# Optimization experiments

Measured on AMD Instinct MI355X. Metric: run time of the kernel, lower is better.

## Reference

```python
import jax, jax.numpy as jnp
import numpy as np


def conv1x1(x, w, b):
    # 1x1 Conv2d: x [B,C,H,W], w [O,C], b [O] -> [B,O,H,W]
    return jnp.einsum('bchw,oc->bohw', x, w) + b[None, :, None, None]


def setup_inputs() -> dict:
    key = jax.random.key(0)
    ks = jax.random.split(key, 10)
    B, C, Ci, H, W = 4, 64, 32, 64, 64
    s = 0.05
    return {
        'supp_feature': jax.random.normal(ks[0], (B, C, H, W), jnp.float32),
        'ref_feature': jax.random.normal(ks[1], (B, C, H, W), jnp.float32),
        'theta_w': jax.random.normal(ks[2], (Ci, C), jnp.float32) * s,
        'theta_b': jax.random.normal(ks[3], (Ci,), jnp.float32) * s,
        'phi_w': jax.random.normal(ks[4], (Ci, C), jnp.float32) * s,
        'phi_b': jax.random.normal(ks[5], (Ci,), jnp.float32) * s,
        'g_w': jax.random.normal(ks[6], (Ci, C), jnp.float32) * s,
        'g_b': jax.random.normal(ks[7], (Ci,), jnp.float32) * s,
        'w_w': jax.random.normal(ks[8], (C, Ci), jnp.float32) * s,
        'w_b': jax.random.normal(ks[9], (C,), jnp.float32) * s,
    }


def reference(supp_feature, ref_feature, theta_w, theta_b, phi_w, phi_b,
              g_w, g_b, w_w, w_b):
    B, C, H, W = supp_feature.shape
    Ci = theta_w.shape[0]
    N = H * W
    theta_x = conv1x1(supp_feature, theta_w, theta_b).reshape(B, Ci, N)  # [B,Ci,N]
    phi_y = conv1x1(ref_feature, phi_w, phi_b).reshape(B, Ci, N)        # [B,Ci,M]
    g_y = conv1x1(ref_feature, g_w, g_b).reshape(B, Ci, N)              # [B,Ci,M]
    # f[b,n,m] = <theta_x[b,:,n], phi_y[b,:,m]>  (unscaled)
    f = jnp.einsum('bcn,bcm->bnm', theta_x, phi_y)
    # NOTE: softmax over dim=1 (the QUERY axis n), matching F.softmax(f, dim=1)
    f_div_C = jax.nn.softmax(f, axis=1)
    # x1[b,c,n] = sum_m f_div_C[b,n,m] * g_y[b,c,m]
    x1 = jnp.einsum('bnm,bcm->bcn', f_div_C, g_y).reshape(B, Ci, H, W)
    z = supp_feature + conv1x1(x1, w_w, w_b)
    return z
```

## Files before the change

### kernel.cpp

```cpp
#include <hip/hip_runtime.h>

#define C_ 64
#define CI_ 32
#define N_ 4096
#define LOG2E 1.4426950408889634f

typedef __attribute__((ext_vector_type(8))) short bf16x8;
typedef __attribute__((ext_vector_type(4))) float f32x4;

__device__ __forceinline__ unsigned short f2bf_rne(float f) {
  unsigned u = __builtin_bit_cast(unsigned, f);
  unsigned r = (u + 0x7FFFu + ((u >> 16) & 1u)) >> 16;
  return (unsigned short)r;
}
__device__ __forceinline__ unsigned pack_bf2(float lo, float hi) {
  unsigned a = (__builtin_bit_cast(unsigned, lo) + 0x8000u) >> 16;
  unsigned b = (__builtin_bit_cast(unsigned, hi) + 0x8000u) & 0xFFFF0000u;
  return a | b;
}
__device__ __forceinline__ float bf2f(unsigned short v) {
  return __builtin_bit_cast(float, (unsigned)v << 16);
}
__device__ __forceinline__ void dma16(const void* gp, const void* lp) {
  __builtin_amdgcn_global_load_lds(
      (const __attribute__((address_space(1))) unsigned*)(unsigned long long)gp,
      (__attribute__((address_space(3))) unsigned*)(unsigned)(unsigned long long)lp,
      16, 0, 0);
}


__global__ __launch_bounds__(256) void k1_proj(
    const float* __restrict__ supp, const float* __restrict__ ref,
    const float* __restrict__ tw, const float* __restrict__ tb,
    const float* __restrict__ pw, const float* __restrict__ pb,
    const float* __restrict__ gw, const float* __restrict__ gb,
    unsigned short* __restrict__ theta, unsigned short* __restrict__ phi2,
    unsigned short* __restrict__ g2)
{
  const int proj = blockIdx.x >> 8;
  const int rr = blockIdx.x & 255;
  const int b = rr >> 6;
  const int n0 = (rr & 63) << 6;
  const int o = __builtin_amdgcn_readfirstlane(threadIdx.x >> 6);
  const int lane = threadIdx.x & 63;
  const int n = n0 + lane;

  const float *W, *bias, *src;
  if (proj == 0)      { W = tw; bias = tb; src = supp; }
  else if (proj == 1) { W = pw; bias = pb; src = ref; }
  else                { W = gw; bias = gb; src = ref; }

  const float* x = src + (size_t)b * (C_ * N_) + n;
  const float* Wo = W + o * 8 * C_;
  float acc[8];
#pragma unroll
  for (int k = 0; k < 8; k++) acc[k] = bias[o * 8 + k];
#pragma unroll 8
  for (int c = 0; c < C_; c++) {
    float v = x[(size_t)c * N_];
#pragma unroll
    for (int k = 0; k < 8; k++) acc[k] = fmaf(Wo[k * C_ + c], v, acc[k]);
  }

  if (proj == 0) {
    unsigned pk[4];
#pragma unroll
    for (int k = 0; k < 4; k++)
      pk[k] = (unsigned)f2bf_rne(acc[2 * k] * LOG2E) |
              ((unsigned)f2bf_rne(acc[2 * k + 1] * LOG2E) << 16);
    *(uint4*)(theta + (((size_t)b * N_ + n) << 5) + o * 8) = *(uint4*)pk;
  } else if (proj == 1) {
    unsigned pk[4];
#pragma unroll
    for (int k = 0; k < 4; k++)
      pk[k] = (unsigned)f2bf_rne(acc[2 * k]) |
              ((unsigned)f2bf_rne(acc[2 * k + 1]) << 16);
    size_t off = (((size_t)b * 128 + (n >> 5)) << 10) + o * 256 + (n & 31) * 8;
    *(uint4*)(phi2 + off) = *(uint4*)pk;
  } else {
    int ml = n & 31;
    int q = (ml & 15) >> 2;
    int j = (ml & 3) | (((ml >> 4) & 1) << 2);
    size_t base = (((size_t)b * 128 + (n >> 5)) << 10) + q * 256 + j;
#pragma unroll
    for (int t = 0; t < 8; t++)
      g2[base + (8 * o + t) * 8] = f2bf_rne(acc[t]);
  }
}

__global__ __launch_bounds__(1024) void k2_den(
    const unsigned short* __restrict__ theta, const unsigned short* __restrict__ phi2,
    float* __restrict__ rden)
{
  const int tid = threadIdx.x;
  const int wave = tid >> 6;
  const int lane = tid & 63;
  const int b = blockIdx.x >> 6;
  const int mbase = (blockIdx.x & 63) << 6;
  const int row16 = lane & 15;
  const int quad = lane >> 4;

  bf16x8 bf[4];
#pragma unroll
  for (int f = 0; f < 4; f++) {
    int ch = (mbase >> 5) + (f >> 1);
    int r = ((f & 1) << 4) + row16;
    bf[f] = *(const bf16x8*)(phi2 +
        (((size_t)b * 128 + ch) << 10) + (quad << 8) + r * 8);
  }

  const unsigned short* abase = theta +
      (((size_t)b * N_ + wave * 256 + row16) << 5) + (quad << 3);

  f32x4 zero = {0.f, 0.f, 0.f, 0.f};
  float dd[16];
#pragma unroll
  for (int k = 0; k < 16; k++) dd[k] = 0.f;

  bf16x8 a0 = *(const bf16x8*)abase;
  bf16x8 a1 = *(const bf16x8*)(abase + 512);
#pragma unroll 2
  for (int it = 0; it < 16; it++) {
    int itn = it + 2 <= 15 ? it + 2 : 15;
    bf16x8 an = *(const bf16x8*)(abase + ((size_t)itn << 9));
#pragma unroll
    for (int f = 0; f < 4; f++) {
      f32x4 ff = __builtin_amdgcn_mfma_f32_16x16x32_bf16(a0, bf[f], zero, 0, 0, 0);
#pragma unroll
      for (int r = 0; r < 4; r++) dd[f * 4 + r] += __builtin_amdgcn_exp2f(ff[r]);
    }
    a0 = a1; a1 = an;
  }

  __shared__ float denp[16][64];
#pragma unroll
  for (int f = 0; f < 4; f++) {
    float v = (dd[f * 4] + dd[f * 4 + 1]) + (dd[f * 4 + 2] + dd[f * 4 + 3]);
    v += __shfl_xor(v, 16);
    v += __shfl_xor(v, 32);
    if (lane < 16) denp[wave][f * 16 + lane] = v;
  }
  __syncthreads();

  if (tid < 64) {
    int p = tid;
    int q = (p >> 3) & 3, j = p & 7;
    int ml = (p & 32) + 4 * q + (j & 3) + ((j >> 2) << 4);
    float den = 0.f;
#pragma unroll
    for (int w = 0; w < 16; w++) den += denp[w][ml];
    rden[(((size_t)b * 128 + (mbase >> 5) + (p >> 5)) << 5) + (p & 31)] = 1.0f / den;
  }
}

__global__ __launch_bounds__(512, 2) void k3_attn(
    const unsigned short* __restrict__ theta, const unsigned short* __restrict__ phi2,
    const unsigned short* __restrict__ g2, const float* __restrict__ rden,
    unsigned short* __restrict__ x1p)
{
  const int tid = threadIdx.x;
  const int w = tid >> 6;
  const int lane = tid & 63;
  const int b = blockIdx.x >> 7;
  const int nt = (blockIdx.x >> 3) & 15;
  const int ms = blockIdx.x & 7;
  const int row16 = lane & 15;
  const int quad = lane >> 4;

  __shared__ __align__(16) unsigned short SB[4 * 2048];

  const int nbase = nt * 256 + w * 32;
  bf16x8 tB0 = *(const bf16x8*)(theta + (((size_t)b * N_ + nbase + row16) << 5) + (quad << 3));
  bf16x8 tB1 = *(const bf16x8*)(theta + (((size_t)b * N_ + nbase + 16 + row16) << 5) + (quad << 3));

  const size_t chunkb = (size_t)b * 128 + ms * 16;

  f32x4 zero = {0.f, 0.f, 0.f, 0.f};
  f32x4 xa0 = zero, xb0 = zero, xa1 = zero, xb1 = zero;

  for (int ph = 0; ph < 4; ph++) {
#pragma unroll
    for (int s = 0; s < 2; s++) {
      int idx = w * 2 + s;
      int c = idx >> 2;
      int a = (idx >> 1) & 1;
      int h = idx & 1;
      const unsigned short* src = (a ? g2 : phi2) +
          ((chunkb + ph * 4 + c) << 10) + (h << 9) + lane * 8;
      const unsigned short* dst = SB + c * 2048 + a * 1024 + h * 512;
      dma16(src, dst);
    }
    __syncthreads();
#pragma unroll
    for (int c = 0; c < 4; c++) {
      const unsigned short* lphi = SB + c * 2048;
      const unsigned short* lg = SB + c * 2048 + 1024;
      bf16x8 pA0 = *(const bf16x8*)(lphi + (quad << 8) + row16 * 8);
      bf16x8 pA1 = *(const bf16x8*)(lphi + (quad << 8) + (row16 + 16) * 8);
      bf16x8 gA0 = *(const bf16x8*)(lg + (quad << 8) + row16 * 8);
      bf16x8 gA1 = *(const bf16x8*)(lg + (quad << 8) + (row16 + 16) * 8);
      const float* rp = rden + ((chunkb + ph * 4 + c) << 5) + (quad << 3);
      f32x4 r0 = *(const f32x4*)rp;
      f32x4 r1 = *(const f32x4*)(rp + 4);

      f32x4 f00 = __builtin_amdgcn_mfma_f32_16x16x32_bf16(pA0, tB0, zero, 0, 0, 0);
      f32x4 f10 = __builtin_amdgcn_mfma_f32_16x16x32_bf16(pA1, tB0, zero, 0, 0, 0);
      f32x4 f01 = __builtin_amdgcn_mfma_f32_16x16x32_bf16(pA0, tB1, zero, 0, 0, 0);
      f32x4 f11 = __builtin_amdgcn_mfma_f32_16x16x32_bf16(pA1, tB1, zero, 0, 0, 0);

      uint4 d0, d1;
      d0.x = pack_bf2(__builtin_amdgcn_exp2f(f00[0]) * r0[0],
                      __builtin_amdgcn_exp2f(f00[1]) * r0[1]);
      d0.y = pack_bf2(__builtin_amdgcn_exp2f(f00[2]) * r0[2],
                      __builtin_amdgcn_exp2f(f00[3]) * r0[3]);
      d0.z = pack_bf2(__builtin_amdgcn_exp2f(f10[0]) * r1[0],
                      __builtin_amdgcn_exp2f(f10[1]) * r1[1]);
      d0.w = pack_bf2(__builtin_amdgcn_exp2f(f10[2]) * r1[2],
                      __builtin_amdgcn_exp2f(f10[3]) * r1[3]);
      d1.x = pack_bf2(__builtin_amdgcn_exp2f(f01[0]) * r0[0],
                      __builtin_amdgcn_exp2f(f01[1]) * r0[1]);
      d1.y = pack_bf2(__builtin_amdgcn_exp2f(f01[2]) * r0[2],
                      __builtin_amdgcn_exp2f(f01[3]) * r0[3]);
      d1.z = pack_bf2(__builtin_amdgcn_exp2f(f11[0]) * r1[0],
                      __builtin_amdgcn_exp2f(f11[1]) * r1[1]);
      d1.w = pack_bf2(__builtin_amdgcn_exp2f(f11[2]) * r1[2],
                      __builtin_amdgcn_exp2f(f11[3]) * r1[3]);
      bf16x8 Pb0 = __builtin_bit_cast(bf16x8, d0);
      bf16x8 Pb1 = __builtin_bit_cast(bf16x8, d1);

      xa0 = __builtin_amdgcn_mfma_f32_16x16x32_bf16(gA0, Pb0, xa0, 0, 0, 0);
      xb0 = __builtin_amdgcn_mfma_f32_16x16x32_bf16(gA1, Pb0, xb0, 0, 0, 0);
      xa1 = __builtin_amdgcn_mfma_f32_16x16x32_bf16(gA0, Pb1, xa1, 0, 0, 0);
      xb1 = __builtin_amdgcn_mfma_f32_16x16x32_bf16(gA1, Pb1, xb1, 0, 0, 0);
    }
    __syncthreads();
  }

  size_t obase = ((size_t)(b * 8 + ms) * CI_) * N_;
#pragma unroll
  for (int r = 0; r < 4; r++) {
    size_t i0 = (size_t)(quad * 4 + r) * N_;
    size_t i1 = (size_t)(16 + quad * 4 + r) * N_;
    x1p[obase + i0 + nbase + row16] = f2bf_rne(xa0[r]);
    x1p[obase + i0 + nbase + 16 + row16] = f2bf_rne(xa1[r]);
    x1p[obase + i1 + nbase + row16] = f2bf_rne(xb0[r]);
    x1p[obase + i1 + nbase + 16 + row16] = f2bf_rne(xb1[r]);
  }
}

__global__ __launch_bounds__(256) void k4_out(
    const unsigned short* __restrict__ x1p, const float* __restrict__ supp,
    const float* __restrict__ ww, const float* __restrict__ wb,
    float* __restrict__ out)
{
  const int tid = threadIdx.x;
  const int b = blockIdx.x >> 7;
  const int n0 = (blockIdx.x & 127) << 5;

  __shared__ float x1L[CI_ * 33];
  __shared__ float wwL[C_ * 33];

  for (int e = tid; e < C_ * CI_; e += 256)
    wwL[(e >> 5) * 33 + (e & 31)] = ww[e];
  for (int e = tid; e < CI_ * 32; e += 256) {
    int i = e >> 5, nl = e & 31;
    size_t a = ((size_t)b * 8 * CI_ + i) * N_ + n0 + nl;
    float s = 0.f;
#pragma unroll
    for (int q = 0; q < 8; q++) s += bf2f(x1p[a + (size_t)q * CI_ * N_]);
    x1L[i * 33 + nl] = s;
  }
  __syncthreads();

  const int c = tid >> 2;
  const int nl0 = (tid & 3) << 3;
  float a[8];
  float bv = wb[c];
#pragma unroll
  for (int j = 0; j < 8; j++) a[j] = bv;
#pragma unroll 8
  for (int i = 0; i < CI_; i++) {
    float wv = wwL[c * 33 + i];
    const float* xr = &x1L[i * 33 + nl0];
#pragma unroll
    for (int j = 0; j < 8; j++) a[j] = fmaf(wv, xr[j], a[j]);
  }
  size_t ob = ((size_t)b * C_ + c) * N_ + n0 + nl0;
  float4 s0 = *(const float4*)(supp + ob);
  float4 s1 = *(const float4*)(supp + ob + 4);
  float4 o0, o1;
  o0.x = a[0] + s0.x; o0.y = a[1] + s0.y; o0.z = a[2] + s0.z; o0.w = a[3] + s0.w;
  o1.x = a[4] + s1.x; o1.y = a[5] + s1.y; o1.z = a[6] + s1.z; o1.w = a[7] + s1.w;
  *(float4*)(out + ob) = o0;
  *(float4*)(out + ob + 4) = o1;
}

extern "C" void kernel_launch(void* const* d_in, const int* in_sizes, int n_in,
                              void* d_out, int out_size, void* d_ws, size_t ws_size,
                              hipStream_t stream)
{
  const float* supp = (const float*)d_in[0];
  const float* ref  = (const float*)d_in[1];
  const float* tw   = (const float*)d_in[2];
  const float* tb   = (const float*)d_in[3];
  const float* pw   = (const float*)d_in[4];
  const float* pb   = (const float*)d_in[5];
  const float* gw   = (const float*)d_in[6];
  const float* gb   = (const float*)d_in[7];
  const float* ww   = (const float*)d_in[8];
  const float* wb   = (const float*)d_in[9];
  float* out = (float*)d_out;

  char* ws = (char*)d_ws;
  unsigned short* theta = (unsigned short*)ws;
  unsigned short* phi2  = (unsigned short*)(ws + (1u << 20));
  unsigned short* g2    = (unsigned short*)(ws + (2u << 20));
  float*          rden  = (float*)(ws + (3u << 20));
  unsigned short* x1p   = (unsigned short*)(ws + (4u << 20));

  hipLaunchKernelGGL(k1_proj, dim3(768), dim3(256), 0, stream,
                     supp, ref, tw, tb, pw, pb, gw, gb, theta, phi2, g2);
  hipLaunchKernelGGL(k2_den, dim3(256), dim3(1024), 0, stream,
                     theta, phi2, rden);
  hipLaunchKernelGGL(k3_attn, dim3(512), dim3(512), 0, stream,
                     theta, phi2, g2, rden, x1p);
  hipLaunchKernelGGL(k4_out, dim3(512), dim3(256), 0, stream,
                     x1p, supp, ww, wb, out);
}
```

Measured before the change: 118.4 us.

## Stage g projection through LDS for vector stores; halve attention block size

In the projection kernel, the g-branch no longer writes scattered 2-byte bf16 values. It stages the fp32 results in shared memory and emits one 16-byte packed store per thread in the swizzled layout. The attention kernel moves from 512-thread blocks covering 256 queries to 256-thread blocks covering 128 queries, doubling the grid and having each wave issue four DMA loads instead of two. The store change targets uncoalesced writes. The block resize trades more redundant phi/g tile loads for finer scheduling granularity and higher blocks-per-CU occupancy.

```diff
diff --git a/kernel.cpp b/kernel.cpp
--- a/kernel.cpp
+++ b/kernel.cpp
@@ -45,6 +45,8 @@
   const int lane = threadIdx.x & 63;
   const int n = n0 + lane;
 
+  __shared__ float gL[CI_][66];
+
   const float *W, *bias, *src;
   if (proj == 0)      { W = tw; bias = tb; src = supp; }
   else if (proj == 1) { W = pw; bias = pb; src = ref; }
@@ -78,13 +80,22 @@
     size_t off = (((size_t)b * 128 + (n >> 5)) << 10) + o * 256 + (n & 31) * 8;
     *(uint4*)(phi2 + off) = *(uint4*)pk;
   } else {
-    int ml = n & 31;
-    int q = (ml & 15) >> 2;
-    int j = (ml & 3) | (((ml >> 4) & 1) << 2);
-    size_t base = (((size_t)b * 128 + (n >> 5)) << 10) + q * 256 + j;
-#pragma unroll
-    for (int t = 0; t < 8; t++)
-      g2[base + (8 * o + t) * 8] = f2bf_rne(acc[t]);
+#pragma unroll
+    for (int k = 0; k < 8; k++) gL[o * 8 + k][lane] = acc[k];
+    __syncthreads();
+    const int t = threadIdx.x;
+    const int c = t >> 7;
+    const int rr2 = t & 127;
+    const int q = rr2 >> 5;
+    const int i = rr2 & 31;
+    const float* g0 = &gL[i][c * 32 + 4 * q];
+    unsigned pk[4];
+    pk[0] = pack_bf2(g0[0], g0[1]);
+    pk[1] = pack_bf2(g0[2], g0[3]);
+    pk[2] = pack_bf2(g0[16], g0[17]);
+    pk[3] = pack_bf2(g0[18], g0[19]);
+    size_t off = (((size_t)b * 128 + (n0 >> 5) + c) << 10) + rr2 * 8;
+    *(uint4*)(g2 + off) = *(uint4*)pk;
   }
 }
 
@@ -153,7 +164,7 @@
   }
 }
 
-__global__ __launch_bounds__(512, 2) void k3_attn(
+__global__ __launch_bounds__(256, 4) void k3_attn(
     const unsigned short* __restrict__ theta, const unsigned short* __restrict__ phi2,
     const unsigned short* __restrict__ g2, const float* __restrict__ rden,
     unsigned short* __restrict__ x1p)
@@ -161,15 +172,15 @@
   const int tid = threadIdx.x;
   const int w = tid >> 6;
   const int lane = tid & 63;
-  const int b = blockIdx.x >> 7;
-  const int nt = (blockIdx.x >> 3) & 15;
+  const int b = blockIdx.x >> 8;
+  const int nt = (blockIdx.x >> 3) & 31;
   const int ms = blockIdx.x & 7;
   const int row16 = lane & 15;
   const int quad = lane >> 4;
 
   __shared__ __align__(16) unsigned short SB[4 * 2048];
 
-  const int nbase = nt * 256 + w * 32;
+  const int nbase = nt * 128 + w * 32;
   bf16x8 tB0 = *(const bf16x8*)(theta + (((size_t)b * N_ + nbase + row16) << 5) + (quad << 3));
   bf16x8 tB1 = *(const bf16x8*)(theta + (((size_t)b * N_ + nbase + 16 + row16) << 5) + (quad << 3));
 
@@ -180,14 +191,13 @@
 
   for (int ph = 0; ph < 4; ph++) {
 #pragma unroll
-    for (int s = 0; s < 2; s++) {
-      int idx = w * 2 + s;
+    for (int s = 0; s < 4; s++) {
+      int idx = w * 4 + s;
       int c = idx >> 2;
-      int a = (idx >> 1) & 1;
-      int h = idx & 1;
-      const unsigned short* src = (a ? g2 : phi2) +
-          ((chunkb + ph * 4 + c) << 10) + (h << 9) + lane * 8;
-      const unsigned short* dst = SB + c * 2048 + a * 1024 + h * 512;
+      int seg = idx & 3;
+      const unsigned short* src = (seg >= 2 ? g2 : phi2) +
+          ((chunkb + ph * 4 + c) << 10) + ((seg & 1) << 9) + lane * 8;
+      const unsigned short* dst = SB + c * 2048 + (seg >= 2 ? 1024 : 0) + ((seg & 1) << 9);
       dma16(src, dst);
     }
     __syncthreads();
@@ -322,7 +332,7 @@
                      supp, ref, tw, tb, pw, pb, gw, gb, theta, phi2, g2);
   hipLaunchKernelGGL(k2_den, dim3(256), dim3(1024), 0, stream,
                      theta, phi2, rden);
-  hipLaunchKernelGGL(k3_attn, dim3(512), dim3(512), 0, stream,
+  hipLaunchKernelGGL(k3_attn, dim3(1024), dim3(256), 0, stream,
                      theta, phi2, g2, rden, x1p);
   hipLaunchKernelGGL(k4_out, dim3(512), dim3(256), 0, stream,
                      x1p, supp, ww, wb, out);
```

Measured after the change: 119.1 us. No clear change (+0.6%).
